# Performance work log

Measured on AMD Instinct MI355X. Metric: run time of the kernel, lower is better.

The kernel has to match this reference:

```python
import jax, jax.numpy as jnp
import numpy as np

STRIDE = 8
D_STATE = 16
D_CONV = 4
DT_RANK = 8
NB = 2            # mamba blocks per direction
B, F_IN, L_IN = 2, 256, 250
F_OUT = 128
KSIZE = 16
L_OUT = (L_IN - 1) * STRIDE + KSIZE   # 2008
D_INNER = 2 * F_OUT                   # 256
LN_EPS = 1e-5


def setup_inputs() -> dict:
    key = jax.random.key(0)
    ks = jax.random.split(key, 12)
    s = 0.05
    return {
        'x': jax.random.normal(ks[0], (B, F_IN, L_IN), jnp.float32),
        'skip': jax.random.normal(ks[1], (B, F_OUT, L_OUT), jnp.float32),
        'res_for': jnp.zeros((1,), jnp.float32),
        'res_back': jnp.zeros((1,), jnp.float32),
        'convT_w': jax.random.normal(ks[2], (F_IN, F_OUT, KSIZE), jnp.float32) * s,
        'convT_b': jnp.zeros((F_OUT,), jnp.float32),
        'fuse_w': jax.random.normal(ks[3], (F_OUT, 2 * F_OUT), jnp.float32) * s,
        'fuse_b': jnp.zeros((F_OUT,), jnp.float32),
        'norm_w': jnp.ones((2, NB, F_OUT), jnp.float32),
        'norm_b': jnp.zeros((2, NB, F_OUT), jnp.float32),
        'in_proj_w': jax.random.normal(ks[4], (2, NB, 2 * D_INNER, F_OUT), jnp.float32) * s,
        'conv_w': jax.random.normal(ks[5], (2, NB, D_INNER, 1, D_CONV), jnp.float32) * s,
        'conv_b': jnp.zeros((2, NB, D_INNER), jnp.float32),
        'x_proj_w': jax.random.normal(ks[6], (2, NB, DT_RANK + 2 * D_STATE, D_INNER), jnp.float32) * s,
        'dt_proj_w': jax.random.normal(ks[7], (2, NB, D_INNER, DT_RANK), jnp.float32) * s,
        'dt_proj_b': jax.random.uniform(ks[8], (2, NB, D_INNER), jnp.float32, -4.0, -2.0),
        'A_log': jnp.broadcast_to(jnp.log(jnp.arange(1, D_STATE + 1, dtype=jnp.float32)), (2, NB, D_INNER, D_STATE)) + jnp.zeros((2, NB, D_INNER, D_STATE), jnp.float32),
        'D_skip': jnp.ones((2, NB, D_INNER), jnp.float32),
        'out_proj_w': jax.random.normal(ks[9], (2, NB, F_OUT, D_INNER), jnp.float32) * s,
    }


def _layernorm(x, w, b):
    mu = x.mean(-1, keepdims=True)
    var = ((x - mu) ** 2).mean(-1, keepdims=True)
    return (x - mu) * jax.lax.rsqrt(var + LN_EPS) * w + b


def _mamba_mixer(x, p):
    # x: [B,L,D] -> [B,L,D]
    Bb, L, _ = x.shape
    xz = jnp.einsum('bld,ed->ble', x, p['in_proj_w'])          # [B,L,2*d_in]
    xc, z = xz[..., :D_INNER], xz[..., D_INNER:]
    # causal depthwise conv1d (pad left d_conv-1)
    conv = jax.lax.conv_general_dilated(
        xc.transpose(0, 2, 1), p['conv_w'], (1,), [(D_CONV - 1, 0)],
        feature_group_count=D_INNER, dimension_numbers=('NCH', 'OIH', 'NCH'))
    xc = jax.nn.silu(conv + p['conv_b'][None, :, None]).transpose(0, 2, 1)  # [B,L,d_in]
    xdbl = jnp.einsum('bld,ed->ble', xc, p['x_proj_w'])        # [B,L,dt_rank+2N]
    dt = xdbl[..., :DT_RANK]
    Bm = xdbl[..., DT_RANK:DT_RANK + D_STATE]                  # [B,L,N]
    Cm = xdbl[..., DT_RANK + D_STATE:]                         # [B,L,N]
    delta = jax.nn.softplus(jnp.einsum('blr,dr->bld', dt, p['dt_proj_w']) + p['dt_proj_b'])
    A = -jnp.exp(p['A_log'])                                   # [d_in,N]

    def step(h, inp):
        d_t, B_t, C_t, u_t = inp                               # [B,d_in],[B,N],[B,N],[B,d_in]
        dA = jnp.exp(d_t[..., None] * A)                       # [B,d_in,N]
        h = dA * h + (d_t * u_t)[..., None] * B_t[:, None, :]
        y = jnp.einsum('bdn,bn->bd', h, C_t)
        return h, y

    h0 = jnp.zeros((Bb, D_INNER, D_STATE), xc.dtype)
    _, ys = jax.lax.scan(step, h0, (delta.transpose(1, 0, 2), Bm.transpose(1, 0, 2),
                                    Cm.transpose(1, 0, 2), xc.transpose(1, 0, 2)))
    y = ys.transpose(1, 0, 2) + xc * p['D_skip']               # [B,L,d_in]
    y = y * jax.nn.silu(z)
    return jnp.einsum('bld,od->blo', y, p['out_proj_w'])


def _mamba_stack(xseq, params, d):
    # prenorm residual blocks, as in mamba_ssm Block (fused_add_norm=False, LayerNorm)
    residual = None
    for i in range(NB):
        p = {k: params[k][d, i] for k in ('norm_w', 'norm_b', 'in_proj_w', 'conv_w', 'conv_b',
                                          'x_proj_w', 'dt_proj_w', 'dt_proj_b', 'A_log', 'D_skip', 'out_proj_w')}
        residual = xseq if residual is None else xseq + residual
        xseq = _mamba_mixer(_layernorm(residual, p['norm_w'], p['norm_b']), p)
    return xseq + residual


def _conv_transpose1d(x, w, b, stride):
    # torch ConvTranspose1d: x [B,Cin,L], w [Cin,Cout,K]
    K = w.shape[-1]
    w_t = jnp.flip(w, -1).transpose(1, 0, 2)                   # [Cout,Cin,K]
    y = jax.lax.conv_general_dilated(x, w_t, (1,), [(K - 1, K - 1)],
                                     lhs_dilation=(stride,),
                                     dimension_numbers=('NCH', 'OIH', 'NCH'))
    return y + b[None, :, None]


def _forward(x, skip, convT_w, convT_b, fuse_w, fuse_b, params):
    h = jax.nn.silu(_conv_transpose1d(x, convT_w, convT_b, STRIDE))
    pad = skip.shape[2] - h.shape[2]
    if pad > 0:
        h = jnp.pad(h, ((0, 0), (0, 0), (0, pad)))
    h = jnp.concatenate([skip, h], axis=1)                     # [B,2*F_OUT,L]
    h = jax.nn.silu(jnp.einsum('bcl,oc->bol', h, fuse_w) + fuse_b[None, :, None])
    xs = h.transpose(0, 2, 1)                                  # [B,L,F_OUT]
    xf = _mamba_stack(xs, params, 0)
    xb = jnp.flip(_mamba_stack(jnp.flip(xs, 1), params, 1), 1)
    return (xf + xb).transpose(0, 2, 1)                        # [B,F_OUT,L]


def reference(x, skip, res_for, res_back, convT_w, convT_b, fuse_w, fuse_b,
              norm_w, norm_b, in_proj_w, conv_w, conv_b, x_proj_w,
              dt_proj_w, dt_proj_b, A_log, D_skip, out_proj_w):
    params = dict(norm_w=norm_w, norm_b=norm_b, in_proj_w=in_proj_w, conv_w=conv_w,
                  conv_b=conv_b, x_proj_w=x_proj_w, dt_proj_w=dt_proj_w, dt_proj_b=dt_proj_b,
                  A_log=A_log, D_skip=D_skip, out_proj_w=out_proj_w)
    return _forward(x, skip, convT_w, convT_b, fuse_w, fuse_b, params)
```

## Files before the change

### kernel.cpp

```cpp
#include <hip/hip_runtime.h>
#include <hip/hip_bf16.h>
#include <math.h>

#define B_    2
#define FIN_  256
#define LIN_  250
#define F_    128
#define K_    16
#define ST_   8
#define L_    2008
#define DI_   256
#define DS_   16
#define RK_   8
#define CV_   4
#define NBLK_ 2
#define NC_   64
#define CL_   32
#define RL_   ((size_t)B_ * L_)

__device__ __forceinline__ float silu_f(float x) {
    return x / (1.f + __expf(-x));
}
__device__ __forceinline__ float softplus_f(float x) {
    return (x > 20.f) ? x : log1pf(__expf(x));
}
__device__ __forceinline__ float dot4(float4 a, float4 b) {
    return a.x * b.x + a.y * b.y + a.z * b.z + a.w * b.w;
}

#define PREP_N (524288 + 32768 + 262144 + 262144 + 65536)
__global__ void prep_k(const float* __restrict__ convT_w, const float* __restrict__ fuse_w,
                       const float* __restrict__ in_proj, const float* __restrict__ out_proj,
                       const float* __restrict__ x_proj,
                       float* __restrict__ W2p, float* __restrict__ fwTp,
                       float* __restrict__ ipTp, float* __restrict__ opTp,
                       float* __restrict__ xpTp) {
    size_t g = (size_t)blockIdx.x * 256 + threadIdx.x;
    if (g >= PREP_N) return;
    if (g < 524288) {
        int ccq = g >> 12, rr = g & 4095;
        int po = rr >> 2, i = rr & 3;
        int cc = ccq * 4 + i;
        int p = po >> 7, o = po & 127;
        int c = cc & 255, k = (cc < 256) ? p : p + 8;
        W2p[g] = convT_w[(size_t)c * 2048 + o * 16 + k];
        return;
    }
    g -= 524288;
    if (g < 32768) {
        int cq = g >> 9, rr = g & 511;
        int o = rr >> 2, i = rr & 3;
        fwTp[g] = fuse_w[(size_t)o * 256 + cq * 4 + i];
        return;
    }
    g -= 32768;
    if (g < 262144) {
        int db = g >> 16, r = g & 65535;
        int cq = r >> 11, rr = r & 2047;
        int e = rr >> 2, i = rr & 3;
        ipTp[g] = in_proj[(size_t)db * 65536 + e * 128 + cq * 4 + i];
        return;
    }
    g -= 262144;
    if (g < 262144) {
        int db = g >> 15, r = g & 32767;
        int cq = r >> 9, rr = r & 511;
        int o = rr >> 2, i = rr & 3;
        opTp[g] = out_proj[(size_t)db * 32768 + o * 256 + cq * 4 + i];
        return;
    }
    g -= 262144;
    {
        int db = g >> 14, r = g & 16383;
        int cq = r >> 8, rr = r & 255;
        int e = rr >> 2, i = rr & 3;
        xpTp[g] = (e < 40) ? x_proj[(size_t)db * 10240 + e * 256 + cq * 4 + i] : 0.f;
    }
}

__global__ void __launch_bounds__(256) convt5_k(
        const float* __restrict__ x, const float* __restrict__ W2p,
        const float* __restrict__ bias, float* __restrict__ hT) {
    int j0 = blockIdx.x * 4, nt = blockIdx.y, b = blockIdx.z;
    int po = nt * 512 + threadIdx.x;
    int p = po >> 7, o = po & 127;

    __shared__ float xr[5][264];

    for (int idx = threadIdx.x; idx < 5 * 256; idx += 256) {
        int i = idx >> 8, c = idx & 255;
        int j = j0 - 1 + i;
        xr[i][c] = (j >= 0 && j < LIN_) ? x[((size_t)b * FIN_ + c) * LIN_ + j] : 0.f;
    }
    __syncthreads();

    float acca[4] = {0.f, 0.f, 0.f, 0.f};
    float accb[4] = {0.f, 0.f, 0.f, 0.f};
    const float4* W4 = (const float4*)W2p;

    for (int ccq = 0; ccq < 64; ++ccq) {
        float4 wa1 = W4[(size_t)ccq * 1024 + po];
        float4 wb1 = W4[(size_t)ccq * 1024 + po + 256];
        float4 wa2 = W4[(size_t)(ccq + 64) * 1024 + po];
        float4 wb2 = W4[(size_t)(ccq + 64) * 1024 + po + 256];
        float4 xv[5];
        #pragma unroll
        for (int i = 0; i < 5; ++i) xv[i] = *(const float4*)&xr[i][ccq * 4];
        #pragma unroll
        for (int jj = 0; jj < 4; ++jj) {
            acca[jj] += dot4(xv[jj + 1], wa1) + dot4(xv[jj], wa2);
            accb[jj] += dot4(xv[jj + 1], wb1) + dot4(xv[jj], wb2);
        }
    }
    float bo = bias[o];
    #pragma unroll
    for (int jj = 0; jj < 4; ++jj) {
        int j = j0 + jj;
        if (j <= 250) {
            hT[((size_t)b * L_ + 8 * j + p) * F_ + o]     = silu_f(acca[jj] + bo);
            hT[((size_t)b * L_ + 8 * j + p + 2) * F_ + o] = silu_f(accb[jj] + bo);
        }
    }
}

__global__ void __launch_bounds__(256) fuse5_k(
        const float* __restrict__ skip, const float* __restrict__ hT,
        const float* __restrict__ fwTp, const float* __restrict__ fb,
        float* __restrict__ xs) {
    int l0 = blockIdx.x * 8, b = blockIdx.y;
    int tid = threadIdx.x;

    __shared__ float ss[8][264];

    for (int idx = tid; idx < 128 * 8; idx += 256) {
        int c = idx >> 3, ll = idx & 7;
        ss[ll][c] = skip[((size_t)b * F_ + c) * L_ + l0 + ll];
    }
    for (int idx = tid; idx < 8 * 128; idx += 256) {
        int ll = idx >> 7, c = idx & 127;
        ss[ll][128 + c] = hT[((size_t)b * L_ + l0 + ll) * F_ + c];
    }
    __syncthreads();

    int o2 = tid & 63, rg = tid >> 6;
    float acca[2] = {0.f, 0.f}, accb[2] = {0.f, 0.f};
    const float4* W4 = (const float4*)fwTp;

    for (int cq = 0; cq < 64; ++cq) {
        float4 wa = W4[cq * 128 + o2];
        float4 wb = W4[cq * 128 + o2 + 64];
        #pragma unroll
        for (int rr = 0; rr < 2; ++rr) {
            float4 s = *(const float4*)&ss[rg * 2 + rr][cq * 4];
            acca[rr] += dot4(s, wa);
            accb[rr] += dot4(s, wb);
        }
    }
    float ba = fb[o2], bb = fb[o2 + 64];
    #pragma unroll
    for (int rr = 0; rr < 2; ++rr) {
        int l = l0 + rg * 2 + rr;
        float va = silu_f(acca[rr] + ba);
        float vb = silu_f(accb[rr] + bb);
        size_t rf = ((size_t)b * L_ + l) * F_;
        size_t rb = (RL_ + (size_t)b * L_ + (L_ - 1 - l)) * F_;
        xs[rf + o2] = va;       xs[rf + o2 + 64] = vb;
        xs[rb + o2] = va;       xs[rb + o2 + 64] = vb;
    }
}

__global__ void __launch_bounds__(256) lndw_k(
        const float* __restrict__ X, const float* __restrict__ nw,
        const float* __restrict__ nb_, const float* __restrict__ ipTp,
        const float* __restrict__ cw, const float* __restrict__ cb,
        const float* __restrict__ xpTp, const float* __restrict__ dtw,
        const float* __restrict__ dtb,
        float* __restrict__ XC, float* __restrict__ XZz,
        float* __restrict__ BCM, float* __restrict__ DELTA, int blk) {
    int rt = blockIdx.x, d = blockIdx.y;
    size_t rbase = (size_t)rt * 8;
    int tid = threadIdx.x, lane = tid & 63, wid = tid >> 6;
    int db = d * NBLK_ + blk;
    size_t dRL = (size_t)d * RL_;

    __shared__ float us[11][132];
    __shared__ float xcs[8][264];
    __shared__ float dts[8][8];

    int wi0 = db * F_;
    for (int r = wid; r < 11; r += 4) {
        long grow = (long)rbase - 3 + r;
        float2 v = make_float2(0.f, 0.f);
        if (grow >= 0)
            v = *(const float2*)(X + (dRL + (size_t)grow) * F_ + lane * 2);
        float s1 = v.x + v.y, s2 = v.x * v.x + v.y * v.y;
        for (int off = 32; off; off >>= 1) {
            s1 += __shfl_xor(s1, off);
            s2 += __shfl_xor(s2, off);
        }
        float mu = s1 * (1.f / F_);
        float var = s2 * (1.f / F_) - mu * mu;
        float rstd = rsqrtf(var + 1e-5f);
        int c2 = lane * 2;
        us[r][c2]     = (v.x - mu) * rstd * nw[wi0 + c2]     + nb_[wi0 + c2];
        us[r][c2 + 1] = (v.y - mu) * rstd * nw[wi0 + c2 + 1] + nb_[wi0 + c2 + 1];
    }
    __syncthreads();

    int o = tid;
    const float4* W4 = (const float4*)(ipTp + (size_t)db * 65536);

    float accx[11], accz[8];
    #pragma unroll
    for (int i = 0; i < 11; ++i) accx[i] = 0.f;
    #pragma unroll
    for (int i = 0; i < 8; ++i) accz[i] = 0.f;
    for (int cq = 0; cq < 32; ++cq) {
        float4 wx = W4[cq * 512 + o];
        float4 wz = W4[cq * 512 + 256 + o];
        #pragma unroll
        for (int r = 0; r < 11; ++r) {
            float4 u = *(const float4*)&us[r][cq * 4];
            accx[r] += dot4(u, wx);
            if (r >= 3) accz[r - 3] += dot4(u, wz);
        }
    }

    {
        int wi = db * DI_ + o;
        float cw0 = cw[(size_t)wi * CV_ + 0], cw1 = cw[(size_t)wi * CV_ + 1];
        float cw2 = cw[(size_t)wi * CV_ + 2], cw3 = cw[(size_t)wi * CV_ + 3];
        float bias = cb[wi];
        #pragma unroll
        for (int r8 = 0; r8 < 8; ++r8) {
            size_t row = rbase + r8;
            int b_r = (row >= L_) ? 1 : 0;
            int l_r = (int)row - b_r * L_;
            int s = r8 + 3;
            float a = bias + accx[s] * cw3;
            if (l_r - 1 >= 0) a += accx[s - 1] * cw2;
            if (l_r - 2 >= 0) a += accx[s - 2] * cw1;
            if (l_r - 3 >= 0) a += accx[s - 3] * cw0;
            float v = silu_f(a);
            xcs[r8][o] = v;
            XC[(dRL + row) * DI_ + o] = v;
            XZz[(dRL + row) * DI_ + o] = accz[r8];
        }
    }
    __syncthreads();

    {
        int e = tid & 63, rg = tid >> 6;
        float acc2[2] = {0.f, 0.f};
        const float4* Wx = (const float4*)(xpTp + (size_t)db * 16384);
        for (int cq = 0; cq < 64; ++cq) {
            float4 w = Wx[cq * 64 + e];
            #pragma unroll
            for (int rr = 0; rr < 2; ++rr)
                acc2[rr] += dot4(*(const float4*)&xcs[rg * 2 + rr][cq * 4], w);
        }
        if (e < RK_) {
            #pragma unroll
            for (int rr = 0; rr < 2; ++rr) dts[rg * 2 + rr][e] = acc2[rr];
        } else if (e < RK_ + 2 * DS_) {
            #pragma unroll
            for (int rr = 0; rr < 2; ++rr) {
                size_t row = rbase + rg * 2 + rr;
                BCM[(dRL + row) * 32 + (e - RK_)] = acc2[rr];
            }
        }
    }
    __syncthreads();

    {
        int wi = db * DI_ + o;
        float dwv[RK_];
        #pragma unroll
        for (int k = 0; k < RK_; ++k) dwv[k] = dtw[(size_t)wi * RK_ + k];
        float bias = dtb[wi];
        #pragma unroll
        for (int rr = 0; rr < 8; ++rr) {
            size_t row = rbase + rr;
            float a = bias;
            #pragma unroll
            for (int k = 0; k < RK_; ++k) a += dts[rr][k] * dwv[k];
            DELTA[(dRL + row) * DI_ + o] = softplus_f(a);
        }
    }
}

__global__ void __launch_bounds__(256) scanA_k(
        float* __restrict__ DELTA, const float* __restrict__ XC,
        const float* __restrict__ BCM, const float* __restrict__ A_log,
        float* __restrict__ Y, float* __restrict__ hpart,
        float* __restrict__ dsum, int blk) {
    int d = blockIdx.z, cnk = blockIdx.y;
    int chunit0 = blockIdx.x * 16;
    int chl = threadIdx.x >> 4, n = threadIdx.x & 15;
    int b = chunit0 >> 8, ch0 = chunit0 & 255;
    int ch = ch0 + chl;
    int t0 = cnk * CL_;
    int nt = L_ - t0; if (nt > CL_) nt = CL_;

    __shared__ float dt_s[CL_][16];
    __shared__ float u_s[CL_][16];
    __shared__ float bc_s[CL_][32];

    size_t rowbase = (size_t)d * RL_ + (size_t)b * L_ + t0;
    for (int idx = threadIdx.x; idx < CL_ * 16; idx += 256) {
        int t = idx >> 4, c = idx & 15;
        float dv = 0.f, uv = 0.f;
        if (t < nt) {
            dv = DELTA[(rowbase + t) * DI_ + ch0 + c];
            uv = XC[(rowbase + t) * DI_ + ch0 + c];
        }
        dt_s[t][c] = dv; u_s[t][c] = uv;
    }
    for (int idx = threadIdx.x; idx < CL_ * 32; idx += 256) {
        int t = idx >> 5, m = idx & 31;
        bc_s[t][m] = (t < nt) ? BCM[(rowbase + t) * 32 + m] : 0.f;
    }
    __syncthreads();

    float A = -__expf(A_log[((size_t)(d * NBLK_ + blk) * DI_ + ch) * DS_ + n]);
    float h = 0.f, cum = 0.f;
    for (int t = 0; t < nt; ++t) {
        float dt = dt_s[t][chl];
        float u  = u_s[t][chl];
        float Bt = bc_s[t][n];
        float Ct = bc_s[t][16 + n];
        cum += dt;
        h = __expf(dt * A) * h + dt * u * Bt;
        float yp = h * Ct;
        yp += __shfl_xor(yp, 1);
        yp += __shfl_xor(yp, 2);
        yp += __shfl_xor(yp, 4);
        yp += __shfl_xor(yp, 8);
        if (n == 0) {
            Y[(rowbase + t) * DI_ + ch] = yp;
            DELTA[(rowbase + t) * DI_ + ch] = cum;
        }
    }
    size_t cb = (size_t)(d * B_ + b) * NC_ + cnk;
    hpart[cb * (DI_ * DS_) + ch * DS_ + n] = h;
    if (n == 0) dsum[cb * DI_ + ch] = cum;
}

__global__ void __launch_bounds__(256) scanB_k(
        float* __restrict__ hpart, const float* __restrict__ dsum,
        const float* __restrict__ A_log, int blk) {
    int chg = blockIdx.x, b = blockIdx.y, d = blockIdx.z;
    int ch0 = chg * 8;
    __shared__ float hs[NC_][8][16];
    __shared__ float ds_s[NC_][8];
    size_t cb0 = (size_t)(d * B_ + b) * NC_;

    for (int idx = threadIdx.x; idx < NC_ * 128; idx += 256) {
        int c = idx >> 7, r = idx & 127;
        hs[c][r >> 4][r & 15] =
            hpart[(cb0 + c) * (DI_ * DS_) + (size_t)(ch0 + (r >> 4)) * DS_ + (r & 15)];
    }
    for (int idx = threadIdx.x; idx < NC_ * 8; idx += 256) {
        int c = idx >> 3, r = idx & 7;
        ds_s[c][r] = dsum[(cb0 + c) * DI_ + ch0 + r];
    }
    __syncthreads();

    if (threadIdx.x < 128) {
        int chl = threadIdx.x >> 4, n = threadIdx.x & 15;
        float A = -__expf(A_log[((size_t)(d * NBLK_ + blk) * DI_ + ch0 + chl) * DS_ + n]);
        float h = 0.f;
        for (int c = 0; c < NC_; ++c) {
            float hc = hs[c][chl][n];
            hs[c][chl][n] = h;
            h = __expf(A * ds_s[c][chl]) * h + hc;
        }
    }
    __syncthreads();

    for (int idx = threadIdx.x; idx < NC_ * 128; idx += 256) {
        int c = idx >> 7, r = idx & 127;
        hpart[(cb0 + c) * (DI_ * DS_) + (size_t)(ch0 + (r >> 4)) * DS_ + (r & 15)] =
            hs[c][r >> 4][r & 15];
    }
}

__global__ void __launch_bounds__(256) gateC_k(
        const float* __restrict__ Y, const float* __restrict__ XC,
        const float* __restrict__ XZz, const float* __restrict__ DELTA ,
        const float* __restrict__ BCM, const float* __restrict__ A_log,
        const float* __restrict__ hcarry, const float* __restrict__ Dsk,
        const float* __restrict__ opTp, const float* __restrict__ resid_in,
        float* __restrict__ outp, int blk) {
    int rt = blockIdx.x, d = blockIdx.y;
    int tid = threadIdx.x;
    size_t rbase = (size_t)rt * 8;
    int db = d * NBLK_ + blk;
    size_t dRL = (size_t)d * RL_;

    __shared__ float yg[8][264];
    __shared__ float Cs[8][16];

    if (tid < 128) {
        int r = tid >> 4, n = tid & 15;
        Cs[r][n] = BCM[(dRL + rbase + r) * 32 + 16 + n];
    }
    __syncthreads();

    {
        int c = tid;
        float Dc = Dsk[(size_t)db * DI_ + c];

        float An[16];
        const float* Ab = A_log + ((size_t)db * DI_ + c) * DS_;
        #pragma unroll
        for (int n = 0; n < 16; ++n) An[n] = -__expf(Ab[n]);

        int b0 = (rbase >= L_) ? 1 : 0;
        int l0 = (int)rbase - b0 * L_;
        int ck0 = l0 >> 5;
        const float* hp0 = hcarry + ((size_t)(d * B_ + b0) * NC_ + ck0) * (DI_ * DS_) + (size_t)c * DS_;
        float K0[16];
        #pragma unroll
        for (int q = 0; q < 4; ++q) {
            float4 v0 = *(const float4*)(hp0 + q * 4);
            K0[4*q] = v0.x; K0[4*q+1] = v0.y; K0[4*q+2] = v0.z; K0[4*q+3] = v0.w;
        }

        #pragma unroll
        for (int r = 0; r < 8; ++r) {
            size_t ri = dRL + rbase + r;
            float cum = DELTA[ri * DI_ + c];
            float corr = 0.f;
            #pragma unroll
            for (int n = 0; n < 16; ++n)
                corr += Cs[r][n] * K0[n] * __expf(An[n] * cum);
            float yv = Y[ri * DI_ + c] + corr;
            float z  = XZz[ri * DI_ + c];
            yg[r][c] = (yv + XC[ri * DI_ + c] * Dc) * silu_f(z);
        }
    }
    __syncthreads();

    int o2 = tid & 63, rg = tid >> 6;
    float acca[2] = {0.f, 0.f};
    float accb[2] = {0.f, 0.f};
    const float4* W4 = (const float4*)(opTp + (size_t)db * 32768);

    for (int cq = 0; cq < 64; ++cq) {
        float4 wa = W4[cq * 128 + o2];
        float4 wb = W4[cq * 128 + o2 + 64];
        #pragma unroll
        for (int rr = 0; rr < 2; ++rr) {
            float4 u = *(const float4*)&yg[rg * 2 + rr][cq * 4];
            acca[rr] += dot4(u, wa);
            accb[rr] += dot4(u, wb);
        }
    }
    #pragma unroll
    for (int rr = 0; rr < 2; ++rr) {
        size_t ri = dRL + rbase + rg * 2 + rr;
        float va = acca[rr], vb = accb[rr];
        if (resid_in) {
            va += resid_in[ri * F_ + o2];
            vb += resid_in[ri * F_ + o2 + 64];
        }
        outp[ri * F_ + o2]      = va;
        outp[ri * F_ + o2 + 64] = vb;
    }
}

__global__ void combine3_k(const float* __restrict__ cur, float* __restrict__ out) {
    int l0 = blockIdx.x * 64, b = blockIdx.y;
    int tid = threadIdx.x;
    __shared__ float s[64][129];
    for (int idx = tid; idx < 64 * 128; idx += 256) {
        int ll = idx >> 7, o = idx & 127;
        int l = l0 + ll;
        if (l < L_) {
            size_t rf = ((size_t)b * L_ + l) * F_ + o;
            size_t rb = (RL_ + (size_t)b * L_ + (L_ - 1 - l)) * F_ + o;
            s[ll][o] = cur[rf] + cur[rb];
        }
    }
    __syncthreads();
    for (int idx = tid; idx < 64 * 128; idx += 256) {
        int o = idx >> 6, ll = idx & 63;
        int l = l0 + ll;
        if (l < L_) out[((size_t)b * F_ + o) * L_ + l] = s[ll][o];
    }
}

extern "C" void kernel_launch(void* const* d_in, const int* in_sizes, int n_in,
                              void* d_out, int out_size, void* d_ws, size_t ws_size,
                              hipStream_t stream) {
    const float* x        = (const float*)d_in[0];
    const float* skip     = (const float*)d_in[1];
    const float* convT_w  = (const float*)d_in[4];
    const float* convT_b  = (const float*)d_in[5];
    const float* fuse_w   = (const float*)d_in[6];
    const float* fuse_b   = (const float*)d_in[7];
    const float* norm_w   = (const float*)d_in[8];
    const float* norm_b   = (const float*)d_in[9];
    const float* in_proj  = (const float*)d_in[10];
    const float* conv_w   = (const float*)d_in[11];
    const float* conv_b   = (const float*)d_in[12];
    const float* x_proj   = (const float*)d_in[13];
    const float* dt_projw = (const float*)d_in[14];
    const float* dt_projb = (const float*)d_in[15];
    const float* A_log    = (const float*)d_in[16];
    const float* D_skip   = (const float*)d_in[17];
    const float* out_proj = (const float*)d_in[18];
    float* out = (float*)d_out;

    float* w = (float*)d_ws;
    size_t off = 0;
    auto alloc = [&](size_t n) { float* p = w + off; off += n; return p; };
    float* hT      = alloc((size_t)B_ * L_ * F_);
    float* W2p     = alloc(524288);
    float* fwTp    = alloc(32768);
    float* ipTp    = alloc(262144);
    float* opTp    = alloc(262144);
    float* xpTp    = alloc(65536);
    float* xs      = alloc(2 * RL_ * F_);
    float* cur     = alloc(2 * RL_ * F_);
    float* res1    = alloc(2 * RL_ * F_);
    float* xzz     = alloc(2 * RL_ * DI_);
    float* xc      = alloc(2 * RL_ * DI_);
    float* dl      = alloc(2 * RL_ * DI_);
    float* bcm     = alloc(2 * RL_ * 32);
    float* yb      = alloc(2 * RL_ * DI_);
    float* hp   = hT;
    float* dsum = cur;
    (void)ws_size; (void)in_sizes; (void)n_in; (void)out_size;

    prep_k<<<(PREP_N + 255) / 256, 256, 0, stream>>>(convT_w, fuse_w, in_proj, out_proj,
                                                     x_proj, W2p, fwTp, ipTp, opTp, xpTp);
    convt5_k<<<dim3(63, 2, 2), 256, 0, stream>>>(x, W2p, convT_b, hT);
    fuse5_k<<<dim3(251, 2), 256, 0, stream>>>(skip, hT, fwTp, fuse_b, xs);

    for (int blk = 0; blk < NBLK_; ++blk) {
        const float* Xin = (blk == 0) ? xs : res1;
        lndw_k<<<dim3(502, 2), 256, 0, stream>>>(Xin, norm_w, norm_b, ipTp,
                                                 conv_w, conv_b, xpTp,
                                                 dt_projw, dt_projb,
                                                 xc, xzz, bcm, dl, blk);
        scanA_k<<<dim3(32, NC_, 2), 256, 0, stream>>>(dl, xc, bcm, A_log, yb, hp, dsum, blk);
        scanB_k<<<dim3(32, B_, 2), 256, 0, stream>>>(hp, dsum, A_log, blk);
        if (blk == 0)
            gateC_k<<<dim3(502, 2), 256, 0, stream>>>(yb, xc, xzz, dl, bcm, A_log, hp,
                                                      D_skip, opTp, xs, res1, 0);
        else
            gateC_k<<<dim3(502, 2), 256, 0, stream>>>(yb, xc, xzz, dl, bcm, A_log, hp,
                                                      D_skip, opTp, res1, cur, 1);
    }

    combine3_k<<<dim3(32, 2), 256, 0, stream>>>(cur, out);
}
```

Baseline: 403.9 us.

## Fold D-skip into scan output and fuse final gate with direction combine

The D*u skip term is now added inside scanA when Y is written, so gateC no longer reads the XC tensor. The last block's gateC is replaced by gateC2, which handles both directions for a tile. It sums the forward and flipped backward outputs in shared memory and writes the transposed result straight to the output, removing the combine kernel and the intermediate cur buffer round trip. The cost is that gateC2 runs half as many blocks, each doing twice the serial work, so parallelism drops.

```diff
diff --git a/kernel.cpp b/kernel.cpp
--- a/kernel.cpp
+++ b/kernel.cpp
@@ -292,6 +292,7 @@
 __global__ void __launch_bounds__(256) scanA_k(
         float* __restrict__ DELTA, const float* __restrict__ XC,
         const float* __restrict__ BCM, const float* __restrict__ A_log,
+        const float* __restrict__ Dsk,
         float* __restrict__ Y, float* __restrict__ hpart,
         float* __restrict__ dsum, int blk) {
     int d = blockIdx.z, cnk = blockIdx.y;
@@ -322,7 +323,9 @@
     }
     __syncthreads();
 
-    float A = -__expf(A_log[((size_t)(d * NBLK_ + blk) * DI_ + ch) * DS_ + n]);
+    int db = d * NBLK_ + blk;
+    float A = -__expf(A_log[((size_t)db * DI_ + ch) * DS_ + n]);
+    float Dch = Dsk[(size_t)db * DI_ + ch];
     float h = 0.f, cum = 0.f;
     for (int t = 0; t < nt; ++t) {
         float dt = dt_s[t][chl];
@@ -337,7 +340,7 @@
         yp += __shfl_xor(yp, 4);
         yp += __shfl_xor(yp, 8);
         if (n == 0) {
-            Y[(rowbase + t) * DI_ + ch] = yp;
+            Y[(rowbase + t) * DI_ + ch] = yp + Dch * u;
             DELTA[(rowbase + t) * DI_ + ch] = cum;
         }
     }
@@ -386,10 +389,9 @@
 }
 
 __global__ void __launch_bounds__(256) gateC_k(
-        const float* __restrict__ Y, const float* __restrict__ XC,
-        const float* __restrict__ XZz, const float* __restrict__ DELTA ,
-        const float* __restrict__ BCM, const float* __restrict__ A_log,
-        const float* __restrict__ hcarry, const float* __restrict__ Dsk,
+        const float* __restrict__ Y, const float* __restrict__ XZz,
+        const float* __restrict__ DELTA , const float* __restrict__ BCM,
+        const float* __restrict__ A_log, const float* __restrict__ hcarry,
         const float* __restrict__ opTp, const float* __restrict__ resid_in,
         float* __restrict__ outp, int blk) {
     int rt = blockIdx.x, d = blockIdx.y;
@@ -409,8 +411,6 @@
 
     {
         int c = tid;
-        float Dc = Dsk[(size_t)db * DI_ + c];
-
         float An[16];
         const float* Ab = A_log + ((size_t)db * DI_ + c) * DS_;
         #pragma unroll
@@ -437,7 +437,7 @@
                 corr += Cs[r][n] * K0[n] * __expf(An[n] * cum);
             float yv = Y[ri * DI_ + c] + corr;
             float z  = XZz[ri * DI_ + c];
-            yg[r][c] = (yv + XC[ri * DI_ + c] * Dc) * silu_f(z);
+            yg[r][c] = yv * silu_f(z);
         }
     }
     __syncthreads();
@@ -460,34 +460,106 @@
     #pragma unroll
     for (int rr = 0; rr < 2; ++rr) {
         size_t ri = dRL + rbase + rg * 2 + rr;
-        float va = acca[rr], vb = accb[rr];
-        if (resid_in) {
-            va += resid_in[ri * F_ + o2];
-            vb += resid_in[ri * F_ + o2 + 64];
-        }
+        float va = acca[rr] + resid_in[ri * F_ + o2];
+        float vb = accb[rr] + resid_in[ri * F_ + o2 + 64];
         outp[ri * F_ + o2]      = va;
         outp[ri * F_ + o2 + 64] = vb;
     }
 }
 
-__global__ void combine3_k(const float* __restrict__ cur, float* __restrict__ out) {
-    int l0 = blockIdx.x * 64, b = blockIdx.y;
+__global__ void __launch_bounds__(256) gateC2_k(
+        const float* __restrict__ Y, const float* __restrict__ XZz,
+        const float* __restrict__ DELTA , const float* __restrict__ BCM,
+        const float* __restrict__ A_log, const float* __restrict__ hcarry,
+        const float* __restrict__ opTp, const float* __restrict__ res1,
+        float* __restrict__ out) {
+    int rt = blockIdx.x;
+    int b = rt / 251, l0 = (rt % 251) * 8;
     int tid = threadIdx.x;
-    __shared__ float s[64][129];
-    for (int idx = tid; idx < 64 * 128; idx += 256) {
-        int ll = idx >> 7, o = idx & 127;
-        int l = l0 + ll;
-        if (l < L_) {
-            size_t rf = ((size_t)b * L_ + l) * F_ + o;
-            size_t rb = (RL_ + (size_t)b * L_ + (L_ - 1 - l)) * F_ + o;
-            s[ll][o] = cur[rf] + cur[rb];
-        }
-    }
-    __syncthreads();
-    for (int idx = tid; idx < 64 * 128; idx += 256) {
-        int o = idx >> 6, ll = idx & 63;
-        int l = l0 + ll;
-        if (l < L_) out[((size_t)b * F_ + o) * L_ + l] = s[ll][o];
+
+    __shared__ float yg[8][264];
+    __shared__ float og[8][132];
+    __shared__ float Cs[2][8][16];
+
+    {
+        int dd = tid >> 7, r = (tid >> 4) & 7, n = tid & 15;
+        int lb = dd ? (L_ - 8 - l0) : l0;
+        size_t row = (size_t)dd * RL_ + (size_t)b * L_ + lb + r;
+        Cs[dd][r][n] = BCM[row * 32 + 16 + n];
+    }
+    __syncthreads();
+
+    for (int dd = 0; dd < 2; ++dd) {
+        int lb = dd ? (L_ - 8 - l0) : l0;
+        size_t rowbase = (size_t)dd * RL_ + (size_t)b * L_ + lb;
+        int db = dd * NBLK_ + 1;
+
+        {
+            int c = tid;
+            float An[16];
+            const float* Ab = A_log + ((size_t)db * DI_ + c) * DS_;
+            #pragma unroll
+            for (int n = 0; n < 16; ++n) An[n] = -__expf(Ab[n]);
+
+            int ck0 = lb >> 5;
+            const float* hp0 = hcarry + ((size_t)(dd * B_ + b) * NC_ + ck0) * (DI_ * DS_) + (size_t)c * DS_;
+            float K0[16];
+            #pragma unroll
+            for (int q = 0; q < 4; ++q) {
+                float4 v0 = *(const float4*)(hp0 + q * 4);
+                K0[4*q] = v0.x; K0[4*q+1] = v0.y; K0[4*q+2] = v0.z; K0[4*q+3] = v0.w;
+            }
+
+            #pragma unroll
+            for (int r = 0; r < 8; ++r) {
+                size_t ri = rowbase + r;
+                float cum = DELTA[ri * DI_ + c];
+                float corr = 0.f;
+                #pragma unroll
+                for (int n = 0; n < 16; ++n)
+                    corr += Cs[dd][r][n] * K0[n] * __expf(An[n] * cum);
+                float yv = Y[ri * DI_ + c] + corr;
+                float z  = XZz[ri * DI_ + c];
+                yg[r][c] = yv * silu_f(z);
+            }
+        }
+        __syncthreads();
+
+        int o2 = tid & 63, rg = tid >> 6;
+        float acca[2] = {0.f, 0.f};
+        float accb[2] = {0.f, 0.f};
+        const float4* W4 = (const float4*)(opTp + (size_t)db * 32768);
+
+        for (int cq = 0; cq < 64; ++cq) {
+            float4 wa = W4[cq * 128 + o2];
+            float4 wb = W4[cq * 128 + o2 + 64];
+            #pragma unroll
+            for (int rr = 0; rr < 2; ++rr) {
+                float4 u = *(const float4*)&yg[rg * 2 + rr][cq * 4];
+                acca[rr] += dot4(u, wa);
+                accb[rr] += dot4(u, wb);
+            }
+        }
+        #pragma unroll
+        for (int rr = 0; rr < 2; ++rr) {
+            int ll = rg * 2 + rr;
+            size_t ri = rowbase + ll;
+            float va = acca[rr] + res1[ri * F_ + o2];
+            float vb = accb[rr] + res1[ri * F_ + o2 + 64];
+            if (dd == 0) {
+                og[ll][o2]      = va;
+                og[ll][o2 + 64] = vb;
+            } else {
+                og[7 - ll][o2]      += va;
+                og[7 - ll][o2 + 64] += vb;
+            }
+        }
+        __syncthreads();
+    }
+
+    for (int idx = tid; idx < 1024; idx += 256) {
+        int o = idx >> 3, ll = idx & 7;
+        out[((size_t)b * F_ + o) * L_ + l0 + ll] = og[ll][o];
     }
 }
 
@@ -539,21 +611,23 @@
     convt5_k<<<dim3(63, 2, 2), 256, 0, stream>>>(x, W2p, convT_b, hT);
     fuse5_k<<<dim3(251, 2), 256, 0, stream>>>(skip, hT, fwTp, fuse_b, xs);
 
-    for (int blk = 0; blk < NBLK_; ++blk) {
-        const float* Xin = (blk == 0) ? xs : res1;
-        lndw_k<<<dim3(502, 2), 256, 0, stream>>>(Xin, norm_w, norm_b, ipTp,
-                                                 conv_w, conv_b, xpTp,
-                                                 dt_projw, dt_projb,
-                                                 xc, xzz, bcm, dl, blk);
-        scanA_k<<<dim3(32, NC_, 2), 256, 0, stream>>>(dl, xc, bcm, A_log, yb, hp, dsum, blk);
-        scanB_k<<<dim3(32, B_, 2), 256, 0, stream>>>(hp, dsum, A_log, blk);
-        if (blk == 0)
-            gateC_k<<<dim3(502, 2), 256, 0, stream>>>(yb, xc, xzz, dl, bcm, A_log, hp,
-                                                      D_skip, opTp, xs, res1, 0);
-        else
-            gateC_k<<<dim3(502, 2), 256, 0, stream>>>(yb, xc, xzz, dl, bcm, A_log, hp,
-                                                      D_skip, opTp, res1, cur, 1);
-    }
-
-    combine3_k<<<dim3(32, 2), 256, 0, stream>>>(cur, out);
-}
+    lndw_k<<<dim3(502, 2), 256, 0, stream>>>(xs, norm_w, norm_b, ipTp,
+                                             conv_w, conv_b, xpTp,
+                                             dt_projw, dt_projb,
+                                             xc, xzz, bcm, dl, 0);
+    scanA_k<<<dim3(32, NC_, 2), 256, 0, stream>>>(dl, xc, bcm, A_log, D_skip,
+                                                  yb, hp, dsum, 0);
+    scanB_k<<<dim3(32, B_, 2), 256, 0, stream>>>(hp, dsum, A_log, 0);
+    gateC_k<<<dim3(502, 2), 256, 0, stream>>>(yb, xzz, dl, bcm, A_log, hp,
+                                              opTp, xs, res1, 0);
+
+    lndw_k<<<dim3(502, 2), 256, 0, stream>>>(res1, norm_w, norm_b, ipTp,
+                                             conv_w, conv_b, xpTp,
+                                             dt_projw, dt_projb,
+                                             xc, xzz, bcm, dl, 1);
+    scanA_k<<<dim3(32, NC_, 2), 256, 0, stream>>>(dl, xc, bcm, A_log, D_skip,
+                                                  yb, hp, dsum, 1);
+    scanB_k<<<dim3(32, B_, 2), 256, 0, stream>>>(hp, dsum, A_log, 1);
+    gateC2_k<<<dim3(502), 256, 0, stream>>>(yb, xzz, dl, bcm, A_log, hp,
+                                            opTp, res1, out);
+}
```

Measured after the change: 399.1 us. No clear change (-1.2%).
